# Kernel tuning notes

Hardware: AMD Instinct MI355X
Metric: run time of the kernel (lower is better)

The kernel has to match this reference:

```python
import jax, jax.numpy as jnp
import numpy as np

NUM_UNITS = 64
NUM_HEADS = 12
MODEL_UNITS = NUM_UNITS * NUM_HEADS  # 768, must equal input feature dim for residual
EPS = 1e-7  # K.epsilon()


def setup_inputs() -> dict:
    key = jax.random.key(0)
    ks = jax.random.split(key, 7)
    B, T, D = 8, 1024, MODEL_UNITS
    x = jax.random.normal(ks[0], (B, T, D), dtype=jnp.float32)
    mask = jnp.ones((B, T), dtype=bool)
    w_q = jax.random.normal(ks[1], (D, MODEL_UNITS), dtype=jnp.float32) * (D ** -0.5)
    w_k = jax.random.normal(ks[2], (D, MODEL_UNITS), dtype=jnp.float32) * (D ** -0.5)
    w_v = jax.random.normal(ks[3], (D, MODEL_UNITS), dtype=jnp.float32) * (D ** -0.5)
    w_final = jax.random.normal(ks[4], (MODEL_UNITS, MODEL_UNITS), dtype=jnp.float32) * (MODEL_UNITS ** -0.5)
    gamma = jnp.ones((MODEL_UNITS,), dtype=jnp.float32)
    beta = jnp.zeros((MODEL_UNITS,), dtype=jnp.float32)
    return {"x": x, "mask": mask, "w_q": w_q, "w_k": w_k, "w_v": w_v,
            "w_final": w_final, "gamma": gamma, "beta": beta}


def reference(x, mask, w_q, w_k, w_v, w_final, gamma, beta):
    B, T, D = x.shape
    H, U = NUM_HEADS, NUM_UNITS
    # Project and split into heads. Keras split(axis=2) -> head h takes cols h*U:(h+1)*U,
    # which is exactly a reshape [B,T,H,U].
    q = (x @ w_q).reshape(B, T, H, U)
    k = (x @ w_k).reshape(B, T, H, U)
    v = (x @ w_v).reshape(B, T, H, U)
    scale = D ** (-0.5)
    # scores: [B,H,T,T]
    scores = jnp.einsum('bthu,bshu->bhts', q, k) * scale
    m = mask.astype(x.dtype)  # [B,T]
    scores = scores * m[:, None, None, :]  # mask keys
    scores = scores * m[:, None, :, None]  # mask queries
    # sum-normalization (NOT softmax), per source
    scores = scores / (jnp.sum(scores, axis=-1, keepdims=True) + EPS)
    out = jnp.einsum('bhts,bshu->bthu', scores, v).reshape(B, T, H * U)
    out = out @ w_final
    out = out + x  # residual
    # faithful reproduction of source 'normalization' (std is assigned mean — source bug)
    mean = jnp.mean(out, axis=-1, keepdims=True)
    std = mean
    out = gamma * (out - mean) / (std + EPS) + beta
    return out
```

## Files before the change

kernel.cpp:

```cpp
#include <hip/hip_runtime.h>

#define NB 8
#define NT 1024
#define ND 768
#define NH 12
#define NU 64
#define BT (NB*NT)
#define SCALE32 ((float)0.03608439182435161)
#define EPS32 1e-7f

__device__ __forceinline__ float dot64_np(const float* a, const float* b)
{
    float r[4];
#pragma unroll
    for (int j = 0; j < 4; j++) r[j] = __fmul_rn(a[j], b[j]);
#pragma unroll
    for (int i = 1; i < 16; i++)
#pragma unroll
        for (int j = 0; j < 4; j++)
            r[j] = __fadd_rn(r[j], __fmul_rn(a[i * 4 + j], b[i * 4 + j]));
    return __fadd_rn(__fadd_rn(r[0], r[2]), __fadd_rn(r[1], r[3]));
}

__global__ __launch_bounds__(256) void mask_k(
    const unsigned char* __restrict__ mb, float* __restrict__ mf)
{
    __shared__ int cntOff, cntAll;
    if (threadIdx.x == 0) { cntOff = 0; cntAll = 0; }
    __syncthreads();
    int lo = 0, la = 0;
    for (int i = threadIdx.x; i < BT; i += 256)
        if (mb[i] != 0) { la++; if ((i & 3) != 0) lo++; }
    atomicAdd(&cntOff, lo);
    atomicAdd(&cntAll, la);
    __syncthreads();
    const bool int32mode = (cntOff == 0) && (cntAll != 0);
    if (int32mode) {
        const int* mi = (const int*)mb;
        for (int i = threadIdx.x; i < BT; i += 256)
            mf[i] = (mi[i] != 0) ? 1.f : 0.f;
    } else {
        for (int i = threadIdx.x; i < BT; i += 256)
            mf[i] = (mb[i] != 0) ? 1.f : 0.f;
    }
}

__global__ __launch_bounds__(256) void gemmseq(
    const float* __restrict__ A, const float* __restrict__ W,
    const float* __restrict__ R, float* __restrict__ C)
{
    __shared__ float sA[64][132];
    __shared__ float sB[64][68];

    const int t = threadIdx.x;
    const int mbase = blockIdx.x * 128;
    const int nbase = blockIdx.y * 64;
    const int m0 = (t >> 4) * 8;
    const int n0 = (t & 15) * 4;

    float acc[8][4], accA[8][4];
#pragma unroll
    for (int i = 0; i < 8; i++)
#pragma unroll
        for (int j = 0; j < 4; j++) { acc[i][j] = 0.f; accA[i][j] = 0.f; }

    for (int k0 = 0; k0 < 768; k0 += 64) {
        __syncthreads();
#pragma unroll
        for (int i = 0; i < 8; i++) {
            const int idx = t + i * 256;
            const int ar = idx >> 4;
            const int ak4 = (idx & 15) * 4;
            const float4 a4 = *(const float4*)&A[(size_t)(mbase + ar) * 768 + k0 + ak4];
            sA[ak4 + 0][ar] = a4.x;
            sA[ak4 + 1][ar] = a4.y;
            sA[ak4 + 2][ar] = a4.z;
            sA[ak4 + 3][ar] = a4.w;
        }
#pragma unroll
        for (int i = 0; i < 4; i++) {
            const int idx = t + i * 256;
            const int br = idx >> 4;
            const int bk4 = (idx & 15) * 4;
            *(float4*)&sB[br][bk4] =
                *(const float4*)&W[(size_t)(k0 + br) * 768 + nbase + bk4];
        }
        __syncthreads();

        for (int kk = 0; kk < 64; kk++) {
            float av[8], bv[4];
            *(float4*)&av[0] = *(const float4*)&sA[kk][m0];
            *(float4*)&av[4] = *(const float4*)&sA[kk][m0 + 4];
            *(float4*)&bv[0] = *(const float4*)&sB[kk][n0];
#pragma unroll
            for (int i = 0; i < 8; i++)
#pragma unroll
                for (int j = 0; j < 4; j++)
                    acc[i][j] = fmaf(av[i], bv[j], acc[i][j]);
        }

        if (k0 + 64 == 384) {
#pragma unroll
            for (int i = 0; i < 8; i++)
#pragma unroll
                for (int j = 0; j < 4; j++) {
                    accA[i][j] = acc[i][j];
                    acc[i][j] = 0.f;
                }
        }
    }

#pragma unroll
    for (int i = 0; i < 8; i++)
#pragma unroll
        for (int j = 0; j < 4; j++) {
            const size_t idx = (size_t)(mbase + m0 + i) * 768 + nbase + n0 + j;
            float o = __fadd_rn(accA[i][j], acc[i][j]);
            if (R) o = __fadd_rn(o, R[idx]);
            C[idx] = o;
        }
}

__global__ __launch_bounds__(128) void denom_np(
    const float* __restrict__ Q, const float* __restrict__ K,
    const float* __restrict__ MF, float* __restrict__ D)
{
    const int bid = blockIdx.x;
    const int lb  = (bid & 7) * 96 + (bid >> 3);
    const int gid = lb * 128 + threadIdx.x;
    const int bh = gid >> 10;
    const int row = gid & 1023;
    const int b = bh / NH, h = bh % NH;
    const int bh_u = __builtin_amdgcn_readfirstlane(bh);
    const int b_u = bh_u / NH, h_u = bh_u % NH;

    const float mq = MF[b * NT + row];

    float qr[64];
    const float4* qp = (const float4*)&Q[((size_t)(b * NT + row)) * ND + h * 64];
#pragma unroll
    for (int i = 0; i < 16; i++) *(float4*)&qr[i * 4] = qp[i];

    const float* Kb = &K[((size_t)(b_u * NT)) * ND + h_u * 64];
    const float* MFb = &MF[b_u * NT];

    float Bi[8];
    for (int c = 0; c < 8; c++) {
        float b8[8];
        for (int s = 0; s < 128; s++) {
            const int sg = c * 128 + s;
            const float dt = dot64_np(qr, Kb + (size_t)sg * ND);
            float sc = __fmul_rn(dt, SCALE32);
            sc = __fmul_rn(sc, MFb[sg]);
            sc = __fmul_rn(sc, mq);
            const int j = s & 7;
            if (s < 8) b8[j] = sc;
            else       b8[j] = __fadd_rn(b8[j], sc);
        }
        Bi[c] = __fadd_rn(__fadd_rn(__fadd_rn(b8[0], b8[1]), __fadd_rn(b8[2], b8[3])),
                          __fadd_rn(__fadd_rn(b8[4], b8[5]), __fadd_rn(b8[6], b8[7])));
    }

    D[(size_t)bh * NT + row] = __fadd_rn(
        __fadd_rn(__fadd_rn(Bi[0], Bi[1]), __fadd_rn(Bi[2], Bi[3])),
        __fadd_rn(__fadd_rn(Bi[4], Bi[5]), __fadd_rn(Bi[6], Bi[7])));
}

__global__ __launch_bounds__(128) void attn_np(
    const float* __restrict__ K, const float* __restrict__ V,
    const float* __restrict__ D, const float* __restrict__ MF,
    float* __restrict__ QA)
{
    const int bid = blockIdx.x;
    const int lb  = (bid & 7) * 96 + (bid >> 3);
    const int gid = lb * 128 + threadIdx.x;
    const int bh = gid >> 10;
    const int row = gid & 1023;
    const int b = bh / NH, h = bh % NH;
    const int bh_u = __builtin_amdgcn_readfirstlane(bh);
    const int b_u = bh_u / NH, h_u = bh_u % NH;

    const float mq = MF[b * NT + row];
    const float De = __fadd_rn(D[(size_t)bh * NT + row], EPS32);

    float qr[64];
    const float4* qp = (const float4*)&QA[((size_t)(b * NT + row)) * ND + h * 64];
#pragma unroll
    for (int i = 0; i < 16; i++) *(float4*)&qr[i * 4] = qp[i];

    float o[64];
#pragma unroll
    for (int j = 0; j < 64; j++) o[j] = 0.f;

    const float* Kb = &K[((size_t)(b_u * NT)) * ND + h_u * 64];
    const float* Vb = &V[((size_t)(b_u * NT)) * ND + h_u * 64];
    const float* MFb = &MF[b_u * NT];

    for (int s = 0; s < NT; s++) {
        const float dt = dot64_np(qr, Kb + (size_t)s * ND);
        float sc = __fmul_rn(dt, SCALE32);
        sc = __fmul_rn(sc, MFb[s]);
        sc = __fmul_rn(sc, mq);
        const float p = __fdiv_rn(sc, De);
        const float* vp = Vb + (size_t)s * ND;
#pragma unroll
        for (int j = 0; j < 64; j++)
            o[j] = __fadd_rn(o[j], __fmul_rn(p, vp[j]));
    }

    float4* op = (float4*)&QA[((size_t)(b * NT + row)) * ND + h * 64];
#pragma unroll
    for (int i = 0; i < 16; i++) op[i] = *(float4*)&o[i * 4];
}

__global__ __launch_bounds__(256) void rownorm_np(
    float* __restrict__ Y, const float* __restrict__ gamma,
    const float* __restrict__ beta)
{
    const int wave = threadIdx.x >> 6, lane = threadIdx.x & 63;
    const int row = blockIdx.x * 4 + wave;
    float* yr = Y + (size_t)row * ND;
    const int c = lane >> 3, j = lane & 7;

    const float* a = yr + c * 96;
    float r = a[j];
#pragma unroll
    for (int i = 1; i < 12; i++) r = __fadd_rn(r, a[i * 8 + j]);

    r = __fadd_rn(r, __shfl_xor(r, 1, 64));
    r = __fadd_rn(r, __shfl_xor(r, 2, 64));
    r = __fadd_rn(r, __shfl_xor(r, 4, 64));
    r = __fadd_rn(r, __shfl_xor(r, 8, 64));
    r = __fadd_rn(r, __shfl_xor(r, 16, 64));
    r = __fadd_rn(r, __shfl_xor(r, 32, 64));

    const float m = __fdiv_rn(r, 768.0f);
    const float mpe = __fadd_rn(m, EPS32);

#pragma unroll
    for (int i = 0; i < 12; i++) {
        const int idx = i * 64 + lane;
        const float v = yr[idx];
        float o = __fsub_rn(v, m);
        o = __fmul_rn(gamma[idx], o);
        o = __fdiv_rn(o, mpe);
        o = __fadd_rn(o, beta[idx]);
        yr[idx] = o;
    }
}

extern "C" void kernel_launch(void* const* d_in, const int* in_sizes, int n_in,
                              void* d_out, int out_size, void* d_ws, size_t ws_size,
                              hipStream_t stream)
{
    (void)in_sizes; (void)n_in; (void)out_size; (void)ws_size;
    const float* x     = (const float*)d_in[0];
    const unsigned char* maskb = (const unsigned char*)d_in[1];
    const float* wq    = (const float*)d_in[2];
    const float* wk    = (const float*)d_in[3];
    const float* wv    = (const float*)d_in[4];
    const float* wf    = (const float*)d_in[5];
    const float* gamma = (const float*)d_in[6];
    const float* beta  = (const float*)d_in[7];

    float* ws = (float*)d_ws;
    float* MF = ws;
    float* D  = MF + BT;
    float* Q  = D + (size_t)96 * NT;
    float* K  = Q + (size_t)BT * ND;
    float* V  = K + (size_t)BT * ND;
    float* Y  = (float*)d_out;

    mask_k<<<1, 256, 0, stream>>>(maskb, MF);
    gemmseq<<<dim3(64, 12), 256, 0, stream>>>(x, wq, nullptr, Q);
    gemmseq<<<dim3(64, 12), 256, 0, stream>>>(x, wk, nullptr, K);
    gemmseq<<<dim3(64, 12), 256, 0, stream>>>(x, wv, nullptr, V);
    denom_np<<<768, 128, 0, stream>>>(Q, K, MF, D);
    attn_np<<<768, 128, 0, stream>>>(K, V, D, MF, Q);
    gemmseq<<<dim3(64, 12), 256, 0, stream>>>(Q, wf, x, Y);
    rownorm_np<<<2048, 256, 0, stream>>>(Y, gamma, beta);
}
```

Before: 1.725 ms.

## Materialize attention scores in the denominator pass and reuse them in attention

The denominator pass now writes every masked, scaled score to a large workspace buffer (all batch-heads × T × T). A new attention kernel reads these stored scores instead of recomputing the 64-wide Q·K dot product for every key. This trades recomputation of the score matrix for a write and a later read of a buffer of roughly 400 MB. The path is taken only when the provided workspace is large enough; otherwise the original kernels run.

```diff
diff --git a/kernel.cpp b/kernel.cpp
--- a/kernel.cpp
+++ b/kernel.cpp
@@ -166,10 +166,10 @@
         __fadd_rn(__fadd_rn(Bi[4], Bi[5]), __fadd_rn(Bi[6], Bi[7])));
 }
 
-__global__ __launch_bounds__(128) void attn_np(
-    const float* __restrict__ K, const float* __restrict__ V,
-    const float* __restrict__ D, const float* __restrict__ MF,
-    float* __restrict__ QA)
+__global__ __launch_bounds__(128) void denom_s(
+    const float* __restrict__ Q, const float* __restrict__ K,
+    const float* __restrict__ MF, float* __restrict__ D,
+    float* __restrict__ S)
 {
     const int bid = blockIdx.x;
     const int lb  = (bid & 7) * 96 + (bid >> 3);
@@ -181,6 +181,54 @@
     const int b_u = bh_u / NH, h_u = bh_u % NH;
 
     const float mq = MF[b * NT + row];
+
+    float qr[64];
+    const float4* qp = (const float4*)&Q[((size_t)(b * NT + row)) * ND + h * 64];
+#pragma unroll
+    for (int i = 0; i < 16; i++) *(float4*)&qr[i * 4] = qp[i];
+
+    const float* Kb = &K[((size_t)(b_u * NT)) * ND + h_u * 64];
+    const float* MFb = &MF[b_u * NT];
+    float* Sb = S + (size_t)bh * NT * NT + row;
+
+    float Bi[8];
+    for (int c = 0; c < 8; c++) {
+        float b8[8];
+        for (int s = 0; s < 128; s++) {
+            const int sg = c * 128 + s;
+            const float dt = dot64_np(qr, Kb + (size_t)sg * ND);
+            float sc = __fmul_rn(dt, SCALE32);
+            sc = __fmul_rn(sc, MFb[sg]);
+            sc = __fmul_rn(sc, mq);
+            Sb[(size_t)sg * NT] = sc;
+            const int j = s & 7;
+            if (s < 8) b8[j] = sc;
+            else       b8[j] = __fadd_rn(b8[j], sc);
+        }
+        Bi[c] = __fadd_rn(__fadd_rn(__fadd_rn(b8[0], b8[1]), __fadd_rn(b8[2], b8[3])),
+                          __fadd_rn(__fadd_rn(b8[4], b8[5]), __fadd_rn(b8[6], b8[7])));
+    }
+
+    D[(size_t)bh * NT + row] = __fadd_rn(
+        __fadd_rn(__fadd_rn(Bi[0], Bi[1]), __fadd_rn(Bi[2], Bi[3])),
+        __fadd_rn(__fadd_rn(Bi[4], Bi[5]), __fadd_rn(Bi[6], Bi[7])));
+}
+
+__global__ __launch_bounds__(128) void attn_np(
+    const float* __restrict__ K, const float* __restrict__ V,
+    const float* __restrict__ D, const float* __restrict__ MF,
+    float* __restrict__ QA)
+{
+    const int bid = blockIdx.x;
+    const int lb  = (bid & 7) * 96 + (bid >> 3);
+    const int gid = lb * 128 + threadIdx.x;
+    const int bh = gid >> 10;
+    const int row = gid & 1023;
+    const int b = bh / NH, h = bh % NH;
+    const int bh_u = __builtin_amdgcn_readfirstlane(bh);
+    const int b_u = bh_u / NH, h_u = bh_u % NH;
+
+    const float mq = MF[b * NT + row];
     const float De = __fadd_rn(D[(size_t)bh * NT + row], EPS32);
 
     float qr[64];
@@ -201,6 +249,42 @@
         float sc = __fmul_rn(dt, SCALE32);
         sc = __fmul_rn(sc, MFb[s]);
         sc = __fmul_rn(sc, mq);
+        const float p = __fdiv_rn(sc, De);
+        const float* vp = Vb + (size_t)s * ND;
+#pragma unroll
+        for (int j = 0; j < 64; j++)
+            o[j] = __fadd_rn(o[j], __fmul_rn(p, vp[j]));
+    }
+
+    float4* op = (float4*)&QA[((size_t)(b * NT + row)) * ND + h * 64];
+#pragma unroll
+    for (int i = 0; i < 16; i++) op[i] = *(float4*)&o[i * 4];
+}
+
+__global__ __launch_bounds__(128) void attn_s(
+    const float* __restrict__ S, const float* __restrict__ V,
+    const float* __restrict__ D, float* __restrict__ QA)
+{
+    const int bid = blockIdx.x;
+    const int lb  = (bid & 7) * 96 + (bid >> 3);
+    const int gid = lb * 128 + threadIdx.x;
+    const int bh = gid >> 10;
+    const int row = gid & 1023;
+    const int b = bh / NH, h = bh % NH;
+    const int bh_u = __builtin_amdgcn_readfirstlane(bh);
+    const int b_u = bh_u / NH, h_u = bh_u % NH;
+
+    const float De = __fadd_rn(D[(size_t)bh * NT + row], EPS32);
+
+    float o[64];
+#pragma unroll
+    for (int j = 0; j < 64; j++) o[j] = 0.f;
+
+    const float* Vb = &V[((size_t)(b_u * NT)) * ND + h_u * 64];
+    const float* Srow = S + (size_t)bh * NT * NT + row;
+
+    for (int s = 0; s < NT; s++) {
+        const float sc = Srow[(size_t)s * NT];
         const float p = __fdiv_rn(sc, De);
         const float* vp = Vb + (size_t)s * ND;
 #pragma unroll
@@ -253,7 +337,7 @@
                               void* d_out, int out_size, void* d_ws, size_t ws_size,
                               hipStream_t stream)
 {
-    (void)in_sizes; (void)n_in; (void)out_size; (void)ws_size;
+    (void)in_sizes; (void)n_in; (void)out_size;
     const float* x     = (const float*)d_in[0];
     const unsigned char* maskb = (const unsigned char*)d_in[1];
     const float* wq    = (const float*)d_in[2];
@@ -269,14 +353,24 @@
     float* Q  = D + (size_t)96 * NT;
     float* K  = Q + (size_t)BT * ND;
     float* V  = K + (size_t)BT * ND;
+    float* S  = V + (size_t)BT * ND;
     float* Y  = (float*)d_out;
+
+    const size_t base_floats = (size_t)BT + (size_t)96 * NT + 3 * (size_t)BT * ND;
+    const size_t need_bytes  = (base_floats + (size_t)96 * NT * NT) * sizeof(float);
+    const bool use_s = (ws_size >= need_bytes);
 
     mask_k<<<1, 256, 0, stream>>>(maskb, MF);
     gemmseq<<<dim3(64, 12), 256, 0, stream>>>(x, wq, nullptr, Q);
     gemmseq<<<dim3(64, 12), 256, 0, stream>>>(x, wk, nullptr, K);
     gemmseq<<<dim3(64, 12), 256, 0, stream>>>(x, wv, nullptr, V);
-    denom_np<<<768, 128, 0, stream>>>(Q, K, MF, D);
-    attn_np<<<768, 128, 0, stream>>>(K, V, D, MF, Q);
+    if (use_s) {
+        denom_s<<<768, 128, 0, stream>>>(Q, K, MF, D, S);
+        attn_s<<<768, 128, 0, stream>>>(S, V, D, Q);
+    } else {
+        denom_np<<<768, 128, 0, stream>>>(Q, K, MF, D);
+        attn_np<<<768, 128, 0, stream>>>(K, V, D, MF, Q);
+    }
     gemmseq<<<dim3(64, 12), 256, 0, stream>>>(Q, wf, x, Y);
     rownorm_np<<<2048, 256, 0, stream>>>(Y, gamma, beta);
 }
```

Result: no change. 1.736 ms (+0.7%).

## Split each attention row across two lanes to double thread count

Applied to the files above, without the earlier changes.

The denominator and attention kernels now assign two lanes to each query row instead of one. Each lane takes half of the key positions (interleaved) and, in attn_np, half of the output columns, exchanging scores via shuffles, and the launch grid doubles to 1536 blocks. The goal is more parallelism and occupancy, plus fewer registers per thread since the accumulator shrinks from 64 to 32. The trade-off is that both lanes still compute the full 64-wide dot product per key, the uniform readfirstlane base pointers are removed, and the shuffle plus branch adds overhead.

```diff
diff --git a/kernel.cpp b/kernel.cpp
--- a/kernel.cpp
+++ b/kernel.cpp
@@ -126,13 +126,13 @@
     const float* __restrict__ MF, float* __restrict__ D)
 {
     const int bid = blockIdx.x;
-    const int lb  = (bid & 7) * 96 + (bid >> 3);
-    const int gid = lb * 128 + threadIdx.x;
-    const int bh = gid >> 10;
-    const int row = gid & 1023;
+    const int lb  = (bid & 7) * 192 + (bid >> 3);
+    const int tid = threadIdx.x;
+    const int rowg = lb * 64 + (tid >> 1);
+    const int p   = tid & 1;
+    const int bh  = rowg >> 10;
+    const int row = rowg & 1023;
     const int b = bh / NH, h = bh % NH;
-    const int bh_u = __builtin_amdgcn_readfirstlane(bh);
-    const int b_u = bh_u / NH, h_u = bh_u % NH;
 
     const float mq = MF[b * NT + row];
 
@@ -141,29 +141,36 @@
 #pragma unroll
     for (int i = 0; i < 16; i++) *(float4*)&qr[i * 4] = qp[i];
 
-    const float* Kb = &K[((size_t)(b_u * NT)) * ND + h_u * 64];
-    const float* MFb = &MF[b_u * NT];
+    const float* Kb  = &K[((size_t)(b * NT)) * ND + h * 64];
+    const float* MFb = &MF[b * NT];
+    const int j0 = 4 * p;
 
     float Bi[8];
     for (int c = 0; c < 8; c++) {
-        float b8[8];
-        for (int s = 0; s < 128; s++) {
-            const int sg = c * 128 + s;
-            const float dt = dot64_np(qr, Kb + (size_t)sg * ND);
-            float sc = __fmul_rn(dt, SCALE32);
-            sc = __fmul_rn(sc, MFb[sg]);
-            sc = __fmul_rn(sc, mq);
-            const int j = s & 7;
-            if (s < 8) b8[j] = sc;
-            else       b8[j] = __fadd_rn(b8[j], sc);
-        }
-        Bi[c] = __fadd_rn(__fadd_rn(__fadd_rn(b8[0], b8[1]), __fadd_rn(b8[2], b8[3])),
-                          __fadd_rn(__fadd_rn(b8[4], b8[5]), __fadd_rn(b8[6], b8[7])));
-    }
-
-    D[(size_t)bh * NT + row] = __fadd_rn(
-        __fadd_rn(__fadd_rn(Bi[0], Bi[1]), __fadd_rn(Bi[2], Bi[3])),
-        __fadd_rn(__fadd_rn(Bi[4], Bi[5]), __fadd_rn(Bi[6], Bi[7])));
+        float b8[4];
+        for (int k = 0; k < 16; k++) {
+#pragma unroll
+            for (int i = 0; i < 4; i++) {
+                const int sg = c * 128 + k * 8 + j0 + i;
+                const float dt = dot64_np(qr, Kb + (size_t)sg * ND);
+                float sc = __fmul_rn(dt, SCALE32);
+                sc = __fmul_rn(sc, MFb[sg]);
+                sc = __fmul_rn(sc, mq);
+                if (k == 0) b8[i] = sc;
+                else        b8[i] = __fadd_rn(b8[i], sc);
+            }
+        }
+        const float half = __fadd_rn(__fadd_rn(b8[0], b8[1]), __fadd_rn(b8[2], b8[3]));
+        const float other = __shfl_xor(half, 1, 64);
+        const float L = (p == 0) ? half : other;
+        const float R = (p == 0) ? other : half;
+        Bi[c] = __fadd_rn(L, R);
+    }
+
+    if (p == 0)
+        D[(size_t)bh * NT + row] = __fadd_rn(
+            __fadd_rn(__fadd_rn(Bi[0], Bi[1]), __fadd_rn(Bi[2], Bi[3])),
+            __fadd_rn(__fadd_rn(Bi[4], Bi[5]), __fadd_rn(Bi[6], Bi[7])));
 }
 
 __global__ __launch_bounds__(128) void attn_np(
@@ -172,13 +179,13 @@
     float* __restrict__ QA)
 {
     const int bid = blockIdx.x;
-    const int lb  = (bid & 7) * 96 + (bid >> 3);
-    const int gid = lb * 128 + threadIdx.x;
-    const int bh = gid >> 10;
-    const int row = gid & 1023;
+    const int lb  = (bid & 7) * 192 + (bid >> 3);
+    const int tid = threadIdx.x;
+    const int rowg = lb * 64 + (tid >> 1);
+    const int p   = tid & 1;
+    const int bh  = rowg >> 10;
+    const int row = rowg & 1023;
     const int b = bh / NH, h = bh % NH;
-    const int bh_u = __builtin_amdgcn_readfirstlane(bh);
-    const int b_u = bh_u / NH, h_u = bh_u % NH;
 
     const float mq = MF[b * NT + row];
     const float De = __fadd_rn(D[(size_t)bh * NT + row], EPS32);
@@ -188,29 +195,37 @@
 #pragma unroll
     for (int i = 0; i < 16; i++) *(float4*)&qr[i * 4] = qp[i];
 
-    float o[64];
-#pragma unroll
-    for (int j = 0; j < 64; j++) o[j] = 0.f;
-
-    const float* Kb = &K[((size_t)(b_u * NT)) * ND + h_u * 64];
-    const float* Vb = &V[((size_t)(b_u * NT)) * ND + h_u * 64];
-    const float* MFb = &MF[b_u * NT];
-
-    for (int s = 0; s < NT; s++) {
-        const float dt = dot64_np(qr, Kb + (size_t)s * ND);
+    float o[32];
+#pragma unroll
+    for (int j = 0; j < 32; j++) o[j] = 0.f;
+
+    const float* Kb   = &K[((size_t)(b * NT)) * ND + h * 64];
+    const float* Vb32 = &V[((size_t)(b * NT)) * ND + h * 64 + 32 * p];
+    const float* MFb  = &MF[b * NT];
+
+    for (int step = 0; step < 512; step++) {
+        const int sme = 2 * step + p;
+        const float dt = dot64_np(qr, Kb + (size_t)sme * ND);
         float sc = __fmul_rn(dt, SCALE32);
-        sc = __fmul_rn(sc, MFb[s]);
+        sc = __fmul_rn(sc, MFb[sme]);
         sc = __fmul_rn(sc, mq);
-        const float p = __fdiv_rn(sc, De);
-        const float* vp = Vb + (size_t)s * ND;
-#pragma unroll
-        for (int j = 0; j < 64; j++)
-            o[j] = __fadd_rn(o[j], __fmul_rn(p, vp[j]));
-    }
-
-    float4* op = (float4*)&QA[((size_t)(b * NT + row)) * ND + h * 64];
-#pragma unroll
-    for (int i = 0; i < 16; i++) op[i] = *(float4*)&o[i * 4];
+        const float pv = __fdiv_rn(sc, De);
+        const float pw = __shfl_xor(pv, 1, 64);
+        const float pe = (p == 0) ? pv : pw;
+        const float po = (p == 0) ? pw : pv;
+        const float* vpe = Vb32 + (size_t)(2 * step) * ND;
+        const float* vpo = vpe + ND;
+#pragma unroll
+        for (int j = 0; j < 32; j++)
+            o[j] = __fadd_rn(o[j], __fmul_rn(pe, vpe[j]));
+#pragma unroll
+        for (int j = 0; j < 32; j++)
+            o[j] = __fadd_rn(o[j], __fmul_rn(po, vpo[j]));
+    }
+
+    float4* op = (float4*)&QA[((size_t)(b * NT + row)) * ND + h * 64 + 32 * p];
+#pragma unroll
+    for (int i = 0; i < 8; i++) op[i] = *(float4*)&o[i * 4];
 }
 
 __global__ __launch_bounds__(256) void rownorm_np(
@@ -275,8 +290,8 @@
     gemmseq<<<dim3(64, 12), 256, 0, stream>>>(x, wq, nullptr, Q);
     gemmseq<<<dim3(64, 12), 256, 0, stream>>>(x, wk, nullptr, K);
     gemmseq<<<dim3(64, 12), 256, 0, stream>>>(x, wv, nullptr, V);
-    denom_np<<<768, 128, 0, stream>>>(Q, K, MF, D);
-    attn_np<<<768, 128, 0, stream>>>(K, V, D, MF, Q);
+    denom_np<<<1536, 128, 0, stream>>>(Q, K, MF, D);
+    attn_np<<<1536, 128, 0, stream>>>(K, V, D, MF, Q);
     gemmseq<<<dim3(64, 12), 256, 0, stream>>>(Q, wf, x, Y);
     rownorm_np<<<2048, 256, 0, stream>>>(Y, gamma, beta);
 }
```

Result: slower. 4.976 ms (+188.5%).

## Fuse denominator and attention kernels, caching scores in per-thread array

Applied to the files above, without the earlier changes.

Merges the separate denominator and attention-apply kernels into one. Each thread keeps its 1024 masked, scaled scores in a private array during the denominator pass and reuses them in the weighted V accumulation, so the Q·K dot products are not recomputed and one launch plus the D buffer are dropped. The 1024-float per-thread array will spill to scratch memory, adding large private-memory traffic and possibly lowering occupancy.

```diff
diff --git a/kernel.cpp b/kernel.cpp
--- a/kernel.cpp
+++ b/kernel.cpp
@@ -121,9 +121,9 @@
         }
 }
 
-__global__ __launch_bounds__(128) void denom_np(
-    const float* __restrict__ Q, const float* __restrict__ K,
-    const float* __restrict__ MF, float* __restrict__ D)
+__global__ __launch_bounds__(128) void attn_fused(
+    const float* __restrict__ K, const float* __restrict__ V,
+    const float* __restrict__ MF, float* __restrict__ QA)
 {
     const int bid = blockIdx.x;
     const int lb  = (bid & 7) * 96 + (bid >> 3);
@@ -137,12 +137,15 @@
     const float mq = MF[b * NT + row];
 
     float qr[64];
-    const float4* qp = (const float4*)&Q[((size_t)(b * NT + row)) * ND + h * 64];
+    const float4* qp = (const float4*)&QA[((size_t)(b * NT + row)) * ND + h * 64];
 #pragma unroll
     for (int i = 0; i < 16; i++) *(float4*)&qr[i * 4] = qp[i];
 
     const float* Kb = &K[((size_t)(b_u * NT)) * ND + h_u * 64];
+    const float* Vb = &V[((size_t)(b_u * NT)) * ND + h_u * 64];
     const float* MFb = &MF[b_u * NT];
+
+    float sarr[NT];
 
     float Bi[8];
     for (int c = 0; c < 8; c++) {
@@ -153,6 +156,7 @@
             float sc = __fmul_rn(dt, SCALE32);
             sc = __fmul_rn(sc, MFb[sg]);
             sc = __fmul_rn(sc, mq);
+            sarr[sg] = sc;
             const int j = s & 7;
             if (s < 8) b8[j] = sc;
             else       b8[j] = __fadd_rn(b8[j], sc);
@@ -160,48 +164,17 @@
         Bi[c] = __fadd_rn(__fadd_rn(__fadd_rn(b8[0], b8[1]), __fadd_rn(b8[2], b8[3])),
                           __fadd_rn(__fadd_rn(b8[4], b8[5]), __fadd_rn(b8[6], b8[7])));
     }
-
-    D[(size_t)bh * NT + row] = __fadd_rn(
+    const float Drow = __fadd_rn(
         __fadd_rn(__fadd_rn(Bi[0], Bi[1]), __fadd_rn(Bi[2], Bi[3])),
         __fadd_rn(__fadd_rn(Bi[4], Bi[5]), __fadd_rn(Bi[6], Bi[7])));
-}
-
-__global__ __launch_bounds__(128) void attn_np(
-    const float* __restrict__ K, const float* __restrict__ V,
-    const float* __restrict__ D, const float* __restrict__ MF,
-    float* __restrict__ QA)
-{
-    const int bid = blockIdx.x;
-    const int lb  = (bid & 7) * 96 + (bid >> 3);
-    const int gid = lb * 128 + threadIdx.x;
-    const int bh = gid >> 10;
-    const int row = gid & 1023;
-    const int b = bh / NH, h = bh % NH;
-    const int bh_u = __builtin_amdgcn_readfirstlane(bh);
-    const int b_u = bh_u / NH, h_u = bh_u % NH;
-
-    const float mq = MF[b * NT + row];
-    const float De = __fadd_rn(D[(size_t)bh * NT + row], EPS32);
-
-    float qr[64];
-    const float4* qp = (const float4*)&QA[((size_t)(b * NT + row)) * ND + h * 64];
-#pragma unroll
-    for (int i = 0; i < 16; i++) *(float4*)&qr[i * 4] = qp[i];
+    const float De = __fadd_rn(Drow, EPS32);
 
     float o[64];
 #pragma unroll
     for (int j = 0; j < 64; j++) o[j] = 0.f;
 
-    const float* Kb = &K[((size_t)(b_u * NT)) * ND + h_u * 64];
-    const float* Vb = &V[((size_t)(b_u * NT)) * ND + h_u * 64];
-    const float* MFb = &MF[b_u * NT];
-
     for (int s = 0; s < NT; s++) {
-        const float dt = dot64_np(qr, Kb + (size_t)s * ND);
-        float sc = __fmul_rn(dt, SCALE32);
-        sc = __fmul_rn(sc, MFb[s]);
-        sc = __fmul_rn(sc, mq);
-        const float p = __fdiv_rn(sc, De);
+        const float p = __fdiv_rn(sarr[s], De);
         const float* vp = Vb + (size_t)s * ND;
 #pragma unroll
         for (int j = 0; j < 64; j++)
@@ -265,8 +238,7 @@
 
     float* ws = (float*)d_ws;
     float* MF = ws;
-    float* D  = MF + BT;
-    float* Q  = D + (size_t)96 * NT;
+    float* Q  = MF + BT;
     float* K  = Q + (size_t)BT * ND;
     float* V  = K + (size_t)BT * ND;
     float* Y  = (float*)d_out;
@@ -275,8 +247,7 @@
     gemmseq<<<dim3(64, 12), 256, 0, stream>>>(x, wq, nullptr, Q);
     gemmseq<<<dim3(64, 12), 256, 0, stream>>>(x, wk, nullptr, K);
     gemmseq<<<dim3(64, 12), 256, 0, stream>>>(x, wv, nullptr, V);
-    denom_np<<<768, 128, 0, stream>>>(Q, K, MF, D);
-    attn_np<<<768, 128, 0, stream>>>(K, V, D, MF, Q);
+    attn_fused<<<768, 128, 0, stream>>>(K, V, MF, Q);
     gemmseq<<<dim3(64, 12), 256, 0, stream>>>(Q, wf, x, Y);
     rownorm_np<<<2048, 256, 0, stream>>>(Y, gamma, beta);
 }
```

Result: no change. 1.752 ms (+1.5%).
